# Kernel optimization log

Hardware: AMD Instinct MI355X
Metric: run time of the kernel (lower is better)

The kernel has to match this reference:

```python
import jax, jax.numpy as jnp
import numpy as np

D_MODEL = 1024
NUM_HEADS = 16
HEAD_DIM = D_MODEL // NUM_HEADS


def setup_inputs() -> dict:
    key = jax.random.key(0)
    ks = jax.random.split(key, 10)
    B, SQ, SKV = 4, 2048, 2048
    s = 1.0 / np.sqrt(D_MODEL)
    return {
        "query": jax.random.normal(ks[0], (B, SQ, D_MODEL), jnp.float32),
        "key_value": jax.random.normal(ks[1], (B, SKV, D_MODEL), jnp.float32),
        "Wq": jax.random.normal(ks[2], (D_MODEL, D_MODEL), jnp.float32) * s,
        "bq": jnp.zeros((D_MODEL,), jnp.float32),
        "Wk": jax.random.normal(ks[3], (D_MODEL, D_MODEL), jnp.float32) * s,
        "bk": jnp.zeros((D_MODEL,), jnp.float32),
        "Wv": jax.random.normal(ks[4], (D_MODEL, D_MODEL), jnp.float32) * s,
        "bv": jnp.zeros((D_MODEL,), jnp.float32),
        "Wo": jax.random.normal(ks[5], (D_MODEL, D_MODEL), jnp.float32) * s,
        "bo": jnp.zeros((D_MODEL,), jnp.float32),
    }


def reference(query, key_value, Wq, bq, Wk, bk, Wv, bv, Wo, bo):
    B, SQ, _ = query.shape
    SKV = key_value.shape[1]
    H, Dh = NUM_HEADS, HEAD_DIM
    # projections (torch Linear: x @ W.T + b); split heads -> (B, H, S, Dh)
    Q = (query @ Wq.T + bq).reshape(B, SQ, H, Dh).transpose(0, 2, 1, 3)
    K = (key_value @ Wk.T + bk).reshape(B, SKV, H, Dh).transpose(0, 2, 1, 3)
    V = (key_value @ Wv.T + bv).reshape(B, SKV, H, Dh).transpose(0, 2, 1, 3)
    scale = jnp.asarray(np.sqrt(Dh), query.dtype)
    scores = jnp.einsum("bhqd,bhkd->bhqk", Q, K) / scale
    weights = jax.nn.softmax(scores, axis=-1)  # dropout is identity in eval
    attn = jnp.einsum("bhqk,bhkd->bhqd", weights, V)
    attn = attn.transpose(0, 2, 1, 3).reshape(B, SQ, H * Dh)
    return attn @ Wo.T + bo
```

## Files before the change

kernel.cpp:

```cpp
#include <hip/hip_runtime.h>

#define NH 16
#define DH 64
#define DM 1024
#define SEQ 2048
#define BATCH 4

typedef short s16x8 __attribute__((ext_vector_type(8)));
typedef float f32x4 __attribute__((ext_vector_type(4)));

__device__ __forceinline__ unsigned short f2bf(float f) {
  union { float f; unsigned int u; } v; v.f = f;
  unsigned int u = v.u;
  unsigned int r = (u + 0x7fffu + ((u >> 16) & 1u)) >> 16;
  return (unsigned short)r;
}

__device__ __forceinline__ unsigned int pkbf(float a, float b) {
#if __has_builtin(__builtin_amdgcn_cvt_pk_bf16_f32)
  typedef short v2s __attribute__((ext_vector_type(2)));
  v2s r = __builtin_amdgcn_cvt_pk_bf16_f32(a, b);
  union { v2s v; unsigned int u; } cv; cv.v = r;
  return cv.u;
#else
  return (unsigned int)f2bf(a) | ((unsigned int)f2bf(b) << 16);
#endif
}

__device__ __forceinline__ float fexp2(float x) {
#if __has_builtin(__builtin_amdgcn_exp2f)
  return __builtin_amdgcn_exp2f(x);
#else
  return exp2f(x);
#endif
}

__device__ __forceinline__ void gload_lds16(const void* g, void* l) {
  __builtin_amdgcn_global_load_lds(
      (const __attribute__((address_space(1))) unsigned int*)g,
      (__attribute__((address_space(3))) unsigned int*)l, 16, 0, 0);
}

__global__ void convert_all(const float* __restrict__ q, const float* __restrict__ kv,
                            const float* __restrict__ w0, const float* __restrict__ w1,
                            const float* __restrict__ w2, const float* __restrict__ w3,
                            unsigned short* __restrict__ oq, unsigned short* __restrict__ okv,
                            unsigned short* __restrict__ ow0, unsigned short* __restrict__ ow1,
                            unsigned short* __restrict__ ow2, unsigned short* __restrict__ ow3) {
  const int NQ4 = (BATCH * SEQ * DM) / 4;
  const int NW4 = (DM * DM) / 4;
  const int total = NQ4 * 2 + NW4 * 4;
  for (int i = blockIdx.x * blockDim.x + threadIdx.x; i < total;
       i += gridDim.x * blockDim.x) {
    const float* s; unsigned short* d; int off;
    if (i < NQ4)            { s = q;  d = oq;  off = i; }
    else if (i < 2 * NQ4)   { s = kv; d = okv; off = i - NQ4; }
    else {
      int j = i - 2 * NQ4; int wsel = j / NW4; off = j - wsel * NW4;
      s = (wsel == 0) ? w0 : (wsel == 1) ? w1 : (wsel == 2) ? w2 : w3;
      d = (wsel == 0) ? ow0 : (wsel == 1) ? ow1 : (wsel == 2) ? ow2 : ow3;
    }
    float4 v = *(const float4*)(s + (size_t)off * 4);
    ushort4 o;
    o.x = f2bf(v.x); o.y = f2bf(v.y); o.z = f2bf(v.z); o.w = f2bf(v.w);
    *(ushort4*)(d + (size_t)off * 4) = o;
  }
}

__device__ __forceinline__ void gemm_tile(const unsigned short* __restrict__ X,
                                          const unsigned short* __restrict__ Wt,
                                          unsigned short* As, unsigned short* Bs,
                                          int m0, int n0, f32x4 (*acc)[4]) {
  const int tid = threadIdx.x;
  const int wv_ = tid >> 6, lane = tid & 63;
  const int quad = lane >> 4, c = lane & 15;
  const int wm = (wv_ >> 1) * 64, wn = (wv_ & 1) * 64;
  const int srow = lane >> 3;
  const int scol = ((lane & 7) ^ srow) * 8;

  for (int kt = 0; kt < DM; kt += 64) {
#pragma unroll
    for (int i = 0; i < 4; ++i) {
      int reg = wv_ * 4 + i;
      gload_lds16(X + (size_t)(m0 + reg * 8 + srow) * DM + kt + scol,
                  (void*)(As + reg * 512));
      gload_lds16(Wt + (size_t)(n0 + reg * 8 + srow) * DM + kt + scol,
                  (void*)(Bs + reg * 512));
    }
    __syncthreads();
#pragma unroll
    for (int k2 = 0; k2 < 2; ++k2) {
      s16x8 a[4], b[4];
      int g = k2 * 4 + quad;
#pragma unroll
      for (int t = 0; t < 4; ++t)
        a[t] = *(const s16x8*)(As + (wm + t * 16 + c) * 64 + ((g ^ (c & 7)) * 8));
#pragma unroll
      for (int t = 0; t < 4; ++t)
        b[t] = *(const s16x8*)(Bs + (wn + t * 16 + c) * 64 + ((g ^ (c & 7)) * 8));
#pragma unroll
      for (int tm = 0; tm < 4; ++tm)
#pragma unroll
        for (int tn = 0; tn < 4; ++tn)
          acc[tm][tn] = __builtin_amdgcn_mfma_f32_16x16x32_bf16(
              a[tm], b[tn], acc[tm][tn], 0, 0, 0);
    }
    __syncthreads();
  }
}

__global__ __launch_bounds__(256)
void gemm_qkv(const unsigned short* __restrict__ Xq,
              const unsigned short* __restrict__ Xkv,
              const unsigned short* __restrict__ W0,
              const unsigned short* __restrict__ W1,
              const unsigned short* __restrict__ W2,
              const float* __restrict__ b0, const float* __restrict__ b1,
              const float* __restrict__ b2,
              unsigned short* __restrict__ OQ, unsigned short* __restrict__ OK_,
              unsigned short* __restrict__ OV) {
  __shared__ alignas(16) unsigned short As[128 * 64];
  __shared__ alignas(16) unsigned short Bs[128 * 64];
  const int m0 = blockIdx.x * 128;
  const int ysel = blockIdx.y >> 3;
  const int n0 = (blockIdx.y & 7) * 128;
  const unsigned short* X = (ysel == 0) ? Xq : Xkv;
  const unsigned short* Wt = (ysel == 0) ? W0 : (ysel == 1) ? W1 : W2;
  const float* bias = (ysel == 0) ? b0 : (ysel == 1) ? b1 : b2;
  unsigned short* Out = (ysel == 0) ? OQ : (ysel == 1) ? OK_ : OV;
  const float scale = (ysel == 0) ? 0.1803368801f : 1.0f;

  f32x4 acc[4][4] = {};
  gemm_tile(X, Wt, As, Bs, m0, n0, acc);

  const int tid = threadIdx.x;
  const int wv_ = tid >> 6, lane = tid & 63;
  const int quad = lane >> 4, c = lane & 15;
  const int wm = (wv_ >> 1) * 64, wn = (wv_ & 1) * 64;
#pragma unroll
  for (int tm = 0; tm < 4; ++tm) {
#pragma unroll
    for (int tn = 0; tn < 4; ++tn) {
      int n = n0 + wn + tn * 16 + c;
      float bv = bias[n];
#pragma unroll
      for (int p = 0; p < 4; ++p) {
        int m = m0 + wm + tm * 16 + quad * 4 + p;
        float val = (acc[tm][tn][p] + bv) * scale;
        int b_ = m >> 11, s_ = m & 2047, h_ = n >> 6, dh = n & 63;
        size_t idx;
        if (ysel < 2) idx = (((size_t)(b_ * NH + h_)) * SEQ + s_) * DH + dh;
        else          idx = (((size_t)(b_ * NH + h_)) * DH + dh) * SEQ + s_;
        Out[idx] = f2bf(val);
      }
    }
  }
}

__global__ __launch_bounds__(256)
void gemm_o(const unsigned short* __restrict__ X,
            const unsigned short* __restrict__ Wt,
            const float* __restrict__ bias, float* __restrict__ Out) {
  __shared__ alignas(16) unsigned short As[128 * 64];
  __shared__ alignas(16) unsigned short Bs[128 * 64];
  const int m0 = blockIdx.x * 128;
  const int n0 = blockIdx.y * 128;
  f32x4 acc[4][4] = {};
  gemm_tile(X, Wt, As, Bs, m0, n0, acc);

  const int tid = threadIdx.x;
  const int wv_ = tid >> 6, lane = tid & 63;
  const int quad = lane >> 4, c = lane & 15;
  const int wm = (wv_ >> 1) * 64, wn = (wv_ & 1) * 64;
#pragma unroll
  for (int tm = 0; tm < 4; ++tm) {
#pragma unroll
    for (int tn = 0; tn < 4; ++tn) {
      int n = n0 + wn + tn * 16 + c;
      float bv = bias[n];
#pragma unroll
      for (int p = 0; p < 4; ++p) {
        int m = m0 + wm + tm * 16 + quad * 4 + p;
        Out[(size_t)m * DM + n] = acc[tm][tn][p] + bv;
      }
    }
  }
}

__global__ __launch_bounds__(256, 4)
void attn_kernel(const unsigned short* __restrict__ Qb,
                 const unsigned short* __restrict__ Kb,
                 const unsigned short* __restrict__ VTb,
                 unsigned short* __restrict__ Ob) {
  __shared__ alignas(16) unsigned short Ks[64 * 64];
  __shared__ alignas(16) unsigned short Vs[64 * 64];
  __shared__ alignas(16) unsigned short Ps[4 * 32 * 68];
  const int tid = threadIdx.x, wv_ = tid >> 6, lane = tid & 63;
  const int quad = lane >> 4, c = lane & 15;
  const int bh = blockIdx.x, qb = blockIdx.y;
  const unsigned short* Qp = Qb + (size_t)bh * SEQ * DH;
  const unsigned short* Kp = Kb + (size_t)bh * SEQ * DH;
  const unsigned short* Vp = VTb + (size_t)bh * DH * SEQ;
  const int wq0 = qb * 128 + wv_ * 32;

  s16x8 aq[2][2];
#pragma unroll
  for (int t = 0; t < 2; ++t)
#pragma unroll
    for (int k2 = 0; k2 < 2; ++k2)
      aq[t][k2] = *(const s16x8*)(Qp + (size_t)(wq0 + t * 16 + c) * DH +
                                  k2 * 32 + quad * 8);

  f32x4 O[2][4] = {};
  float lsum[2][4] = {};

  const int srow = lane >> 3;
  const int schunk = ((lane & 7) ^ srow);
  unsigned short* Pw = Ps + wv_ * 32 * 68;

  for (int kt = 0; kt < SEQ; kt += 64) {
    __syncthreads();
#pragma unroll
    for (int i = 0; i < 2; ++i) {
      int reg = wv_ * 2 + i;
      gload_lds16(Kp + (size_t)(kt + reg * 8 + srow) * DH + schunk * 8,
                  (void*)(Ks + reg * 512));
      gload_lds16(Vp + (size_t)(reg * 8 + srow) * SEQ + kt + schunk * 8,
                  (void*)(Vs + reg * 512));
    }
    __syncthreads();

    f32x4 s[2][4] = {};
#pragma unroll
    for (int k2 = 0; k2 < 2; ++k2) {
      s16x8 bk[4];
#pragma unroll
      for (int j = 0; j < 4; ++j)
        bk[j] = *(const s16x8*)(Ks + (j * 16 + c) * 64 +
                                (((k2 * 4 + quad) ^ (c & 7)) * 8));
#pragma unroll
      for (int t = 0; t < 2; ++t)
#pragma unroll
        for (int j = 0; j < 4; ++j)
          s[t][j] = __builtin_amdgcn_mfma_f32_16x16x32_bf16(aq[t][k2], bk[j],
                                                            s[t][j], 0, 0, 0);
    }

#pragma unroll
    for (int t = 0; t < 2; ++t) {
#pragma unroll
      for (int j = 0; j < 4; ++j) {
        float e0 = fexp2(s[t][j][0]);
        float e1 = fexp2(s[t][j][1]);
        float e2 = fexp2(s[t][j][2]);
        float e3 = fexp2(s[t][j][3]);
        lsum[t][0] += e0; lsum[t][1] += e1;
        lsum[t][2] += e2; lsum[t][3] += e3;
        unsigned int w01 = pkbf(e0, e1);
        unsigned int w23 = pkbf(e2, e3);
        int rbase = t * 16 + quad * 4;
        int col = j * 16 + c;
        Pw[(rbase + 0) * 68 + col] = (unsigned short)w01;
        Pw[(rbase + 1) * 68 + col] = (unsigned short)(w01 >> 16);
        Pw[(rbase + 2) * 68 + col] = (unsigned short)w23;
        Pw[(rbase + 3) * 68 + col] = (unsigned short)(w23 >> 16);
      }
    }

#pragma unroll
    for (int k2h = 0; k2h < 2; ++k2h) {
      s16x8 ap[2];
#pragma unroll
      for (int t = 0; t < 2; ++t)
        ap[t] = *(const s16x8*)(Pw + (size_t)(t * 16 + c) * 68 +
                                k2h * 32 + quad * 8);
      int g = k2h * 4 + quad;
#pragma unroll
      for (int nv = 0; nv < 4; ++nv) {
        s16x8 bv = *(const s16x8*)(Vs + (nv * 16 + c) * 64 + ((g ^ (c & 7)) * 8));
#pragma unroll
        for (int t = 0; t < 2; ++t)
          O[t][nv] = __builtin_amdgcn_mfma_f32_16x16x32_bf16(ap[t], bv,
                                                             O[t][nv], 0, 0, 0);
      }
    }
  }

  const int b_ = bh >> 4, h_ = bh & 15;
#pragma unroll
  for (int t = 0; t < 2; ++t) {
#pragma unroll
    for (int p = 0; p < 4; ++p) {
      float l = lsum[t][p];
      l += __shfl_xor(l, 1);
      l += __shfl_xor(l, 2);
      l += __shfl_xor(l, 4);
      l += __shfl_xor(l, 8);
      float inv = 1.0f / l;
      int s_ = wq0 + t * 16 + quad * 4 + p;
#pragma unroll
      for (int nv = 0; nv < 4; ++nv) {
        Ob[((size_t)(b_ * SEQ + s_)) * DM + h_ * 64 + nv * 16 + c] =
            f2bf(O[t][nv][p] * inv);
      }
    }
  }
}

extern "C" void kernel_launch(void* const* d_in, const int* in_sizes, int n_in,
                              void* d_out, int out_size, void* d_ws, size_t ws_size,
                              hipStream_t stream) {
  const float* q  = (const float*)d_in[0];
  const float* kv = (const float*)d_in[1];
  const float* Wq = (const float*)d_in[2];
  const float* bq = (const float*)d_in[3];
  const float* Wk = (const float*)d_in[4];
  const float* bk = (const float*)d_in[5];
  const float* Wv = (const float*)d_in[6];
  const float* bv = (const float*)d_in[7];
  const float* Wo = (const float*)d_in[8];
  const float* bo = (const float*)d_in[9];

  char* ws = (char*)d_ws;
  const size_t MB = 1024 * 1024;
  unsigned short* q_bf  = (unsigned short*)(ws);
  unsigned short* kv_bf = (unsigned short*)(ws + 16 * MB);
  unsigned short* wq_bf = (unsigned short*)(ws + 32 * MB);
  unsigned short* wk_bf = (unsigned short*)(ws + 34 * MB);
  unsigned short* wv_bf = (unsigned short*)(ws + 36 * MB);
  unsigned short* wo_bf = (unsigned short*)(ws + 38 * MB);
  unsigned short* Qb    = (unsigned short*)(ws + 40 * MB);
  unsigned short* Kb    = (unsigned short*)(ws + 56 * MB);
  unsigned short* VTb   = (unsigned short*)(ws + 72 * MB);
  unsigned short* attn  = (unsigned short*)(ws + 88 * MB);

  convert_all<<<2048, 256, 0, stream>>>(q, kv, Wq, Wk, Wv, Wo,
                                        q_bf, kv_bf, wq_bf, wk_bf, wv_bf, wo_bf);
  gemm_qkv<<<dim3(64, 24), 256, 0, stream>>>(q_bf, kv_bf, wq_bf, wk_bf, wv_bf,
                                             bq, bk, bv, Qb, Kb, VTb);
  attn_kernel<<<dim3(64, 16), 256, 0, stream>>>(Qb, Kb, VTb, attn);
  gemm_o<<<dim3(64, 8), 256, 0, stream>>>(attn, wo_bf, bo, (float*)d_out);
}
```

Before: 366.0 us.

## Double-buffer K/V tiles and keep softmax probabilities in registers via transposed MFMA

```diff
diff --git a/kernel.cpp b/kernel.cpp
--- a/kernel.cpp
+++ b/kernel.cpp
@@ -143,15 +143,25 @@
     for (int tn = 0; tn < 4; ++tn) {
       int n = n0 + wn + tn * 16 + c;
       float bv = bias[n];
-#pragma unroll
-      for (int p = 0; p < 4; ++p) {
-        int m = m0 + wm + tm * 16 + quad * 4 + p;
-        float val = (acc[tm][tn][p] + bv) * scale;
-        int b_ = m >> 11, s_ = m & 2047, h_ = n >> 6, dh = n & 63;
-        size_t idx;
-        if (ysel < 2) idx = (((size_t)(b_ * NH + h_)) * SEQ + s_) * DH + dh;
-        else          idx = (((size_t)(b_ * NH + h_)) * DH + dh) * SEQ + s_;
-        Out[idx] = f2bf(val);
+      int m_base = m0 + wm + tm * 16 + quad * 4;
+      if (ysel == 2) {
+        int b_ = m_base >> 11, s_ = m_base & 2047, h_ = n >> 6, dh = n & 63;
+        size_t idx = (((size_t)(b_ * NH + h_)) * DH + dh) * SEQ + s_;
+        ushort4 o4;
+        o4.x = f2bf(acc[tm][tn][0] + bv);
+        o4.y = f2bf(acc[tm][tn][1] + bv);
+        o4.z = f2bf(acc[tm][tn][2] + bv);
+        o4.w = f2bf(acc[tm][tn][3] + bv);
+        *(ushort4*)(&Out[idx]) = o4;
+      } else {
+#pragma unroll
+        for (int p = 0; p < 4; ++p) {
+          int m = m_base + p;
+          float val = (acc[tm][tn][p] + bv) * scale;
+          int b_ = m >> 11, s_ = m & 2047, h_ = n >> 6, dh = n & 63;
+          size_t idx = (((size_t)(b_ * NH + h_)) * SEQ + s_) * DH + dh;
+          Out[idx] = f2bf(val);
+        }
       }
     }
   }
@@ -192,9 +202,8 @@
                  const unsigned short* __restrict__ Kb,
                  const unsigned short* __restrict__ VTb,
                  unsigned short* __restrict__ Ob) {
-  __shared__ alignas(16) unsigned short Ks[64 * 64];
-  __shared__ alignas(16) unsigned short Vs[64 * 64];
-  __shared__ alignas(16) unsigned short Ps[4 * 32 * 68];
+  __shared__ alignas(16) unsigned short SM[16384];
+
   const int tid = threadIdx.x, wv_ = tid >> 6, lane = tid & 63;
   const int quad = lane >> 4, c = lane & 15;
   const int bh = blockIdx.x, qb = blockIdx.y;
@@ -211,99 +220,125 @@
       aq[t][k2] = *(const s16x8*)(Qp + (size_t)(wq0 + t * 16 + c) * DH +
                                   k2 * 32 + quad * 8);
 
-  f32x4 O[2][4] = {};
-  float lsum[2][4] = {};
+  f32x4 ot[4][2] = {};
+  float lsum[2] = {};
 
   const int srow = lane >> 3;
-  const int schunk = ((lane & 7) ^ srow);
-  unsigned short* Pw = Ps + wv_ * 32 * 68;
+  const int schunk = (lane & 7) ^ srow;
+
+#pragma unroll
+  for (int i = 0; i < 2; ++i) {
+    int reg = wv_ * 2 + i;
+    gload_lds16(Kp + (size_t)(reg * 8 + srow) * DH + schunk * 8,
+                (void*)(SM + reg * 512));
+    gload_lds16(Vp + (size_t)(reg * 8 + srow) * SEQ + schunk * 8,
+                (void*)(SM + 8192 + reg * 512));
+  }
 
   for (int kt = 0; kt < SEQ; kt += 64) {
+    const int cur = (kt >> 6) & 1;
     __syncthreads();
-#pragma unroll
-    for (int i = 0; i < 2; ++i) {
-      int reg = wv_ * 2 + i;
-      gload_lds16(Kp + (size_t)(kt + reg * 8 + srow) * DH + schunk * 8,
-                  (void*)(Ks + reg * 512));
-      gload_lds16(Vp + (size_t)(reg * 8 + srow) * SEQ + kt + schunk * 8,
-                  (void*)(Vs + reg * 512));
-    }
-    __syncthreads();
-
-    f32x4 s[2][4] = {};
+    if (kt + 64 < SEQ) {
+      const int nxt = cur ^ 1;
+#pragma unroll
+      for (int i = 0; i < 2; ++i) {
+        int reg = wv_ * 2 + i;
+        gload_lds16(Kp + (size_t)(kt + 64 + reg * 8 + srow) * DH + schunk * 8,
+                    (void*)(SM + nxt * 4096 + reg * 512));
+        gload_lds16(Vp + (size_t)(reg * 8 + srow) * SEQ + kt + 64 + schunk * 8,
+                    (void*)(SM + 8192 + nxt * 4096 + reg * 512));
+      }
+    }
+    const unsigned short* K_ = SM + cur * 4096;
+    const unsigned short* V_ = SM + 8192 + cur * 4096;
+
+    f32x4 s[2][2][2] = {};
 #pragma unroll
     for (int k2 = 0; k2 < 2; ++k2) {
-      s16x8 bk[4];
-#pragma unroll
-      for (int j = 0; j < 4; ++j)
-        bk[j] = *(const s16x8*)(Ks + (j * 16 + c) * 64 +
-                                (((k2 * 4 + quad) ^ (c & 7)) * 8));
+      s16x8 ak[2][2];
+#pragma unroll
+      for (int jp = 0; jp < 2; ++jp)
+#pragma unroll
+        for (int h = 0; h < 2; ++h) {
+          int r = jp * 32 + ((c >> 2) << 3) + h * 4 + (c & 3);
+          int g = k2 * 4 + quad;
+          ak[jp][h] = *(const s16x8*)(K_ + r * 64 + ((g ^ (r & 7)) * 8));
+        }
 #pragma unroll
       for (int t = 0; t < 2; ++t)
 #pragma unroll
-        for (int j = 0; j < 4; ++j)
-          s[t][j] = __builtin_amdgcn_mfma_f32_16x16x32_bf16(aq[t][k2], bk[j],
-                                                            s[t][j], 0, 0, 0);
-    }
-
-#pragma unroll
-    for (int t = 0; t < 2; ++t) {
-#pragma unroll
-      for (int j = 0; j < 4; ++j) {
-        float e0 = fexp2(s[t][j][0]);
-        float e1 = fexp2(s[t][j][1]);
-        float e2 = fexp2(s[t][j][2]);
-        float e3 = fexp2(s[t][j][3]);
-        lsum[t][0] += e0; lsum[t][1] += e1;
-        lsum[t][2] += e2; lsum[t][3] += e3;
-        unsigned int w01 = pkbf(e0, e1);
-        unsigned int w23 = pkbf(e2, e3);
-        int rbase = t * 16 + quad * 4;
-        int col = j * 16 + c;
-        Pw[(rbase + 0) * 68 + col] = (unsigned short)w01;
-        Pw[(rbase + 1) * 68 + col] = (unsigned short)(w01 >> 16);
-        Pw[(rbase + 2) * 68 + col] = (unsigned short)w23;
-        Pw[(rbase + 3) * 68 + col] = (unsigned short)(w23 >> 16);
-      }
-    }
-
-#pragma unroll
-    for (int k2h = 0; k2h < 2; ++k2h) {
-      s16x8 ap[2];
-#pragma unroll
-      for (int t = 0; t < 2; ++t)
-        ap[t] = *(const s16x8*)(Pw + (size_t)(t * 16 + c) * 68 +
-                                k2h * 32 + quad * 8);
-      int g = k2h * 4 + quad;
-#pragma unroll
-      for (int nv = 0; nv < 4; ++nv) {
-        s16x8 bv = *(const s16x8*)(Vs + (nv * 16 + c) * 64 + ((g ^ (c & 7)) * 8));
+        for (int jp = 0; jp < 2; ++jp)
+#pragma unroll
+          for (int h = 0; h < 2; ++h)
+            s[t][jp][h] = __builtin_amdgcn_mfma_f32_16x16x32_bf16(
+                ak[jp][h], aq[t][k2], s[t][jp][h], 0, 0, 0);
+    }
+
+    s16x8 bp[2][2];
+#pragma unroll
+    for (int t = 0; t < 2; ++t)
+#pragma unroll
+      for (int jp = 0; jp < 2; ++jp) {
+        float e00 = fexp2(s[t][jp][0][0]);
+        float e01 = fexp2(s[t][jp][0][1]);
+        float e02 = fexp2(s[t][jp][0][2]);
+        float e03 = fexp2(s[t][jp][0][3]);
+        float e10 = fexp2(s[t][jp][1][0]);
+        float e11 = fexp2(s[t][jp][1][1]);
+        float e12 = fexp2(s[t][jp][1][2]);
+        float e13 = fexp2(s[t][jp][1][3]);
+        lsum[t] += ((e00 + e01) + (e02 + e03)) + ((e10 + e11) + (e12 + e13));
+        union { s16x8 v; unsigned int u[4]; } pk;
+        pk.u[0] = pkbf(e00, e01);
+        pk.u[1] = pkbf(e02, e03);
+        pk.u[2] = pkbf(e10, e11);
+        pk.u[3] = pkbf(e12, e13);
+        bp[t][jp] = pk.v;
+      }
+
+#pragma unroll
+    for (int jp = 0; jp < 2; ++jp)
+#pragma unroll
+      for (int dt = 0; dt < 4; ++dt) {
+        int g = jp * 4 + quad;
+        int r = dt * 16 + c;
+        s16x8 av = *(const s16x8*)(V_ + r * 64 + ((g ^ (r & 7)) * 8));
 #pragma unroll
         for (int t = 0; t < 2; ++t)
-          O[t][nv] = __builtin_amdgcn_mfma_f32_16x16x32_bf16(ap[t], bv,
-                                                             O[t][nv], 0, 0, 0);
-      }
-    }
-  }
-
+          ot[dt][t] = __builtin_amdgcn_mfma_f32_16x16x32_bf16(
+              av, bp[t][jp], ot[dt][t], 0, 0, 0);
+      }
+  }
+
+#pragma unroll
+  for (int t = 0; t < 2; ++t) {
+    lsum[t] += __shfl_xor(lsum[t], 16);
+    lsum[t] += __shfl_xor(lsum[t], 32);
+  }
+
+  __syncthreads();
+
+  unsigned short* Lq = SM + wv_ * (32 * 72);
+#pragma unroll
+  for (int t = 0; t < 2; ++t) {
+    float inv = 1.0f / lsum[t];
+#pragma unroll
+    for (int dt = 0; dt < 4; ++dt) {
+      unsigned int w01 = pkbf(ot[dt][t][0] * inv, ot[dt][t][1] * inv);
+      unsigned int w23 = pkbf(ot[dt][t][2] * inv, ot[dt][t][3] * inv);
+      unsigned short* p = Lq + (t * 16 + c) * 72 + dt * 16 + quad * 4;
+      *(unsigned int*)(p) = w01;
+      *(unsigned int*)(p + 2) = w23;
+    }
+  }
   const int b_ = bh >> 4, h_ = bh & 15;
-#pragma unroll
-  for (int t = 0; t < 2; ++t) {
-#pragma unroll
-    for (int p = 0; p < 4; ++p) {
-      float l = lsum[t][p];
-      l += __shfl_xor(l, 1);
-      l += __shfl_xor(l, 2);
-      l += __shfl_xor(l, 4);
-      l += __shfl_xor(l, 8);
-      float inv = 1.0f / l;
-      int s_ = wq0 + t * 16 + quad * 4 + p;
-#pragma unroll
-      for (int nv = 0; nv < 4; ++nv) {
-        Ob[((size_t)(b_ * SEQ + s_)) * DM + h_ * 64 + nv * 16 + c] =
-            f2bf(O[t][nv][p] * inv);
-      }
-    }
+  const int ql = lane >> 1, hf = lane & 1;
+  const unsigned short* Lr = Lq + ql * 72 + hf * 32;
+  unsigned short* Og = Ob + ((size_t)(b_ * SEQ + wq0 + ql)) * DM + h_ * 64 + hf * 32;
+#pragma unroll
+  for (int j = 0; j < 4; ++j) {
+    s16x8 v = *(const s16x8*)(Lr + j * 8);
+    *(s16x8*)(Og + j * 8) = v;
   }
 }
 
```

Measured after the change: 327.3 us. 1.12x faster.
